# Kernel tuning notes

Measured on AMD Instinct MI355X. Metric: run time of the kernel, lower is better.

Reference implementation:

```python
import jax, jax.numpy as jnp
import numpy as np

N = 100000   # nodes
E = 3200000  # edges
CIN = 6
H = 256
G = 16       # graphs in batch
EPS = 1e-5


def setup_inputs() -> dict:
    key = jax.random.key(0)
    ks = jax.random.split(key, 16)
    inp = {
        'pos': jax.random.normal(ks[0], (N, 3), dtype=jnp.float32),
        'norm': jax.random.normal(ks[1], (N, 3), dtype=jnp.float32),
        'edge_index': jax.random.randint(ks[2], (2, E), 0, N, dtype=jnp.int64),
        'batch': jnp.sort(jax.random.randint(ks[3], (N,), 0, G, dtype=jnp.int64)),
        'bn0_g': jnp.ones((CIN,), jnp.float32), 'bn0_b': jnp.zeros((CIN,), jnp.float32),
    }
    dims = [(CIN, H), (H, H), (H, H), (H, H)]
    for i, (ci, co) in enumerate(dims, start=1):
        inp[f'W{i}'] = jax.random.normal(ks[3 + i], (ci, co), jnp.float32) * 0.05
        inp[f'b{i}'] = jnp.zeros((co,), jnp.float32)
        inp[f'bn{i}_g'] = jnp.ones((co,), jnp.float32)
        inp[f'bn{i}_b'] = jnp.zeros((co,), jnp.float32)
    return inp


def _bn(x, g, b):
    # BatchNorm1d, training mode: biased batch stats over node dim
    m = jnp.mean(x, axis=0)
    v = jnp.var(x, axis=0)
    return (x - m) * jax.lax.rsqrt(v + EPS) * g + b


def _gcn(x, W, bias, row, col, en, sl):
    # GCNConv: linear -> symmetric-normalized aggregation (with self loops) -> +bias
    xw = x @ W                                             # [N, C_out]
    agg = jax.ops.segment_sum(en[:, None] * xw[row], col, num_segments=N)
    return agg + sl[:, None] * xw + bias


def reference(pos, norm, edge_index, batch,
              bn0_g, bn0_b,
              W1, b1, bn1_g, bn1_b,
              W2, b2, bn2_g, bn2_b,
              W3, b3, bn3_g, bn3_b,
              W4, b4, bn4_g, bn4_b):
    row, col = edge_index[0], edge_index[1]
    # gcn_norm with self loops: deg includes +1 self loop weight
    deg = jax.ops.segment_sum(jnp.ones((E,), jnp.float32), col, num_segments=N) + 1.0
    dinv = jax.lax.rsqrt(deg)
    en = dinv[row] * dinv[col]   # edge norm
    sl = dinv * dinv             # self-loop norm

    x = jnp.concatenate([pos, norm], axis=1)   # [N, 6]
    x = _bn(x, bn0_g, bn0_b)
    for (W, b, g, be) in [(W1, b1, bn1_g, bn1_b), (W2, b2, bn2_g, bn2_b),
                          (W3, b3, bn3_g, bn3_b), (W4, b4, bn4_g, bn4_b)]:
        x = _bn(jax.nn.relu(_gcn(x, W, b, row, col, en, sl)), g, be)

    # global mean pool over graph ids
    sums = jax.ops.segment_sum(x, batch, num_segments=G)
    cnt = jax.ops.segment_sum(jnp.ones((N,), jnp.float32), batch, num_segments=G)
    return sums / jnp.maximum(cnt, 1.0)[:, None]
```

## Files before the change

### kernel.cpp

```cpp
#include <hip/hip_runtime.h>
#include <hip/hip_bf16.h>
#include <cstdint>

#define N_NODES 100000
#define NPAD    100032
#define N_EDGES 3200000
#define HID 256
#define NG 16
#define BN_EPS 1e-5f
#define B0 120
#define PB 1024
#define SROWS ((N_NODES + PB - 1) / PB)
#define PBR 128
#define RPR (PB / PBR)
#define FPART 25000

typedef unsigned short u16;
using bf16x8 = __attribute__((ext_vector_type(8))) short;
using f32x4  = __attribute__((ext_vector_type(4))) float;

__device__ __forceinline__ float bf2f(u16 b) {
    return __uint_as_float(((unsigned)b) << 16);
}
__device__ __forceinline__ u16 f2bf(float f) {
    unsigned u = __float_as_uint(f);
    unsigned r = (u + 0x7FFFu + ((u >> 16) & 1u)) >> 16;
    return (u16)r;
}
__device__ __forceinline__ float4 ld_bf16x4(const u16* p) {
    ushort4 u = *reinterpret_cast<const ushort4*>(p);
    float4 f;
    f.x = bf2f(u.x); f.y = bf2f(u.y); f.z = bf2f(u.z); f.w = bf2f(u.w);
    return f;
}

__global__ void k_count(const int* __restrict__ coli, int* __restrict__ cnt) {
    int i = blockIdx.x * blockDim.x + threadIdx.x;
    int st = gridDim.x * blockDim.x;
    for (; i < N_EDGES; i += st) atomicAdd(&cnt[coli[i]], 1);
}

__global__ void k_scan(const int* __restrict__ cnt, int* __restrict__ ptr,
                       int* __restrict__ ptr2, float* __restrict__ dinv) {
    __shared__ int wsum[16];
    const int t = threadIdx.x;
    const int wv = t >> 6;
    const int ln = t & 63;
    int carry = 0;
    for (int base = 0; base < N_NODES; base += 4096) {
        int idx = base + t * 4;
        int v0 = 0, v1 = 0, v2 = 0, v3 = 0;
        if (idx + 3 < N_NODES) {
            int4 q = *reinterpret_cast<const int4*>(&cnt[idx]);
            v0 = q.x; v1 = q.y; v2 = q.z; v3 = q.w;
        } else {
            if (idx + 0 < N_NODES) v0 = cnt[idx + 0];
            if (idx + 1 < N_NODES) v1 = cnt[idx + 1];
            if (idx + 2 < N_NODES) v2 = cnt[idx + 2];
        }
        if (idx + 0 < N_NODES) dinv[idx + 0] = rsqrtf((float)v0 + 1.0f);
        if (idx + 1 < N_NODES) dinv[idx + 1] = rsqrtf((float)v1 + 1.0f);
        if (idx + 2 < N_NODES) dinv[idx + 2] = rsqrtf((float)v2 + 1.0f);
        if (idx + 3 < N_NODES) dinv[idx + 3] = rsqrtf((float)v3 + 1.0f);
        int s = v0 + v1 + v2 + v3;
        int sc = s;
        for (int off = 1; off < 64; off <<= 1) {
            int u = __shfl_up(sc, off);
            if (ln >= off) sc += u;
        }
        if (ln == 63) wsum[wv] = sc;
        __syncthreads();
        if (wv == 0 && ln < 16) {
            int a = wsum[ln];
            for (int off = 1; off < 16; off <<= 1) {
                int u = __shfl_up(a, off, 16);
                if (ln >= off) a += u;
            }
            wsum[ln] = a;
        }
        __syncthreads();
        int total = wsum[15];
        int excl = carry + (wv ? wsum[wv - 1] : 0) + sc - s;
        if (idx + 0 < N_NODES) { ptr[idx + 0] = excl; ptr2[idx + 0] = excl; } excl += v0;
        if (idx + 1 < N_NODES) { ptr[idx + 1] = excl; ptr2[idx + 1] = excl; } excl += v1;
        if (idx + 2 < N_NODES) { ptr[idx + 2] = excl; ptr2[idx + 2] = excl; } excl += v2;
        if (idx + 3 < N_NODES) { ptr[idx + 3] = excl; ptr2[idx + 3] = excl; }
        __syncthreads();
        carry += total;
    }
    if (t == 0) ptr[N_NODES] = carry;
}

__global__ void k_fillp(const int* __restrict__ rowi, const int* __restrict__ coli,
                        int* __restrict__ ptr2, int* __restrict__ esrc, int lo) {
    int i = blockIdx.x * blockDim.x + threadIdx.x;
    int st = gridDim.x * blockDim.x;
    const int hi = lo + FPART;
    for (; i < N_EDGES; i += st) {
        int c = coli[i];
        if (c >= lo && c < hi) {
            int p = atomicAdd(&ptr2[c], 1);
            esrc[p] = rowi[i];
        }
    }
}

__global__ __launch_bounds__(256) void k_batchcnt(const int* __restrict__ batch,
                                                  int* __restrict__ cg) {
    __shared__ int h[NG];
    if (threadIdx.x < NG) h[threadIdx.x] = 0;
    __syncthreads();
    int i = blockIdx.x * blockDim.x + threadIdx.x;
    if (i < N_NODES) atomicAdd(&h[batch[i]], 1);
    __syncthreads();
    if (threadIdx.x < NG) {
        int v = h[threadIdx.x];
        if (v) atomicAdd(&cg[threadIdx.x], v);
    }
}

__global__ __launch_bounds__(256) void k_bn0stats(const float* __restrict__ pos,
                                                  const float* __restrict__ nrm,
                                                  float* __restrict__ part ) {
    float s[6] = {0, 0, 0, 0, 0, 0}, q[6] = {0, 0, 0, 0, 0, 0};
    int i = blockIdx.x * blockDim.x + threadIdx.x;
    int stp = gridDim.x * blockDim.x;
    for (; i < N_NODES; i += stp) {
        float v;
        v = pos[i * 3 + 0]; s[0] += v; q[0] += v * v;
        v = pos[i * 3 + 1]; s[1] += v; q[1] += v * v;
        v = pos[i * 3 + 2]; s[2] += v; q[2] += v * v;
        v = nrm[i * 3 + 0]; s[3] += v; q[3] += v * v;
        v = nrm[i * 3 + 1]; s[4] += v; q[4] += v * v;
        v = nrm[i * 3 + 2]; s[5] += v; q[5] += v * v;
    }
#pragma unroll
    for (int k = 0; k < 6; ++k) {
        for (int o = 32; o > 0; o >>= 1) { s[k] += __shfl_down(s[k], o); q[k] += __shfl_down(q[k], o); }
    }
    __shared__ float ls[4][12];
    const int wv = threadIdx.x >> 6;
    const int ln = threadIdx.x & 63;
    if (ln == 0) {
#pragma unroll
        for (int k = 0; k < 6; ++k) { ls[wv][k] = s[k]; ls[wv][6 + k] = q[k]; }
    }
    __syncthreads();
    if (threadIdx.x < 12)
        part[blockIdx.x * 12 + threadIdx.x] =
            ls[0][threadIdx.x] + ls[1][threadIdx.x] + ls[2][threadIdx.x] + ls[3][threadIdx.x];
}

__global__ void k_fold6(const float* __restrict__ W,
                        const float* __restrict__ part, float invcnt,
                        const float* __restrict__ gamma, const float* __restrict__ beta,
                        float* __restrict__ Wf, float* __restrict__ rvB) {
    __shared__ float st[12];
    int c = threadIdx.x;
    if (c < 12) {
        float a = 0.f;
        for (int b = 0; b < B0; ++b) a += part[b * 12 + c];
        st[c] = a;
    }
    __syncthreads();
    float acc = 0.f;
    for (int k = 0; k < 6; ++k) {
        float m = st[k] * invcnt;
        float var = st[6 + k] * invcnt - m * m;
        float A = gamma[k] * rsqrtf(var + BN_EPS);
        float B = beta[k] - m * A;
        float w = W[k * HID + c];
        Wf[k * HID + c] = A * w;
        acc = fmaf(B, w, acc);
    }
    rvB[c] = acc;
}

__global__ __launch_bounds__(256) void k_reduce(const float* __restrict__ part,
                                                float* __restrict__ red) {
    const int b = blockIdx.x;
    const int t = threadIdx.x;
    float a0 = 0.f, a1 = 0.f;
#pragma unroll
    for (int r = 0; r < RPR; ++r) {
        const float* p = &part[(size_t)(b * RPR + r) * 512];
        a0 += p[t];
        a1 += p[t + 256];
    }
    red[(size_t)b * 512 + t] = a0;
    red[(size_t)b * 512 + 256 + t] = a1;
}

__global__ void k_fold256(const float* __restrict__ W,
                          const float* __restrict__ red , float invcnt,
                          const float* __restrict__ gamma, const float* __restrict__ beta,
                          u16* __restrict__ WhiT, u16* __restrict__ WloT,
                          float* __restrict__ rv) {
    __shared__ float ss[HID], sq[HID];
    int c = threadIdx.x;
    {
        float a = 0.f, b = 0.f;
#pragma unroll 4
        for (int bb = 0; bb < PBR; ++bb) {
            a += red[bb * 512 + c];
            b += red[bb * 512 + HID + c];
        }
        ss[c] = a; sq[c] = b;
    }
    __syncthreads();
    float acc = 0.f;
    for (int k = 0; k < HID; ++k) {
        float m = ss[k] * invcnt;
        float var = sq[k] * invcnt - m * m;
        float A = gamma[k] * rsqrtf(var + BN_EPS);
        float B = beta[k] - m * A;
        float w = W[k * HID + c];
        float wf = A * w;
        u16 hi = f2bf(wf);
        WhiT[c * HID + k] = hi;
        WloT[c * HID + k] = f2bf(wf - bf2f(hi));
        acc = fmaf(B, w, acc);
    }
    rv[c] = acc;
}

__global__ __launch_bounds__(256) void k_agg6(
    const float* __restrict__ pos, const float* __restrict__ nrm,
    const int* __restrict__ ptr, const int* __restrict__ esrc,
    const float* __restrict__ dinv, float* __restrict__ z) {
    const int wv = threadIdx.x >> 6;
    const int ln = threadIdx.x & 63;
    const int n = blockIdx.x * 4 + wv;
    const float dn = dinv[n];
    float z0 = 0, z1 = 0, z2 = 0, z3 = 0, z4 = 0, z5 = 0, t = 0;
    const int s_ = ptr[n], e_ = ptr[n + 1];
    for (int e = s_ + ln; e < e_; e += 64) {
        int src = esrc[e];
        float w = dn * dinv[src];
        z0 = fmaf(w, pos[src * 3 + 0], z0);
        z1 = fmaf(w, pos[src * 3 + 1], z1);
        z2 = fmaf(w, pos[src * 3 + 2], z2);
        z3 = fmaf(w, nrm[src * 3 + 0], z3);
        z4 = fmaf(w, nrm[src * 3 + 1], z4);
        z5 = fmaf(w, nrm[src * 3 + 2], z5);
        t += w;
    }
    if (ln == 0) {
        float sl = dn * dn;
        z0 = fmaf(sl, pos[n * 3 + 0], z0);
        z1 = fmaf(sl, pos[n * 3 + 1], z1);
        z2 = fmaf(sl, pos[n * 3 + 2], z2);
        z3 = fmaf(sl, nrm[n * 3 + 0], z3);
        z4 = fmaf(sl, nrm[n * 3 + 1], z4);
        z5 = fmaf(sl, nrm[n * 3 + 2], z5);
        t += sl;
    }
#pragma unroll
    for (int o = 1; o < 64; o <<= 1) {
        z0 += __shfl_xor(z0, o); z1 += __shfl_xor(z1, o); z2 += __shfl_xor(z2, o);
        z3 += __shfl_xor(z3, o); z4 += __shfl_xor(z4, o); z5 += __shfl_xor(z5, o);
        t  += __shfl_xor(t, o);
    }
    if (ln == 0) {
        *reinterpret_cast<f32x4*>(&z[n * 8])     = f32x4{z0, z1, z2, z3};
        *reinterpret_cast<f32x4*>(&z[n * 8 + 4]) = f32x4{z4, z5, t, 0.f};
    }
}

__global__ __launch_bounds__(256) void k_gemm1b(
    const float* __restrict__ z, const float* __restrict__ Wf,
    const float* __restrict__ rvB, const float* __restrict__ b1,
    u16* __restrict__ out) {
    const int c = threadIdx.x;
    float w0 = Wf[0 * HID + c], w1 = Wf[1 * HID + c], w2 = Wf[2 * HID + c];
    float w3 = Wf[3 * HID + c], w4 = Wf[4 * HID + c], w5 = Wf[5 * HID + c];
    const float rvc = rvB[c], bc = b1[c];
    for (int n = blockIdx.x; n < N_NODES; n += gridDim.x) {
        float x0 = z[n * 8 + 0], x1 = z[n * 8 + 1], x2 = z[n * 8 + 2];
        float x3 = z[n * 8 + 3], x4 = z[n * 8 + 4], x5 = z[n * 8 + 5];
        float s  = z[n * 8 + 6];
        float acc = fmaf(s, rvc, bc);
        acc = fmaf(x0, w0, acc); acc = fmaf(x1, w1, acc); acc = fmaf(x2, w2, acc);
        acc = fmaf(x3, w3, acc); acc = fmaf(x4, w4, acc); acc = fmaf(x5, w5, acc);
        out[(size_t)n * HID + c] = f2bf(fmaxf(acc, 0.f));
    }
}

__global__ __launch_bounds__(256) void k_gemm_mfma(
    const u16* __restrict__ X, const u16* __restrict__ WhiT,
    const u16* __restrict__ WloT, const float* __restrict__ rv,
    u16* __restrict__ out) {
    const int tid = threadIdx.x;
    const int wv = tid >> 6;
    const int ln = tid & 63;
    const int row0 = blockIdx.x * 64;
    const int lr = ln & 15;
    const int lk = (ln >> 4) * 8;
    const int wcol0 = wv * 64;

    f32x4 acc[4][4] = {};
    for (int kk = 0; kk < HID; kk += 32) {
        bf16x8 a[4], bh[4], bl[4];
#pragma unroll
        for (int i = 0; i < 4; ++i) {
            int r = row0 + i * 16 + lr;
            a[i] = *reinterpret_cast<const bf16x8*>(&X[(size_t)r * HID + kk + lk]);
        }
#pragma unroll
        for (int c = 0; c < 4; ++c) {
            int col = wcol0 + c * 16 + lr;
            bh[c] = *reinterpret_cast<const bf16x8*>(&WhiT[(size_t)col * HID + kk + lk]);
            bl[c] = *reinterpret_cast<const bf16x8*>(&WloT[(size_t)col * HID + kk + lk]);
        }
#pragma unroll
        for (int i = 0; i < 4; ++i)
#pragma unroll
            for (int c = 0; c < 4; ++c) {
                acc[i][c] = __builtin_amdgcn_mfma_f32_16x16x32_bf16(a[i], bh[c], acc[i][c], 0, 0, 0);
                acc[i][c] = __builtin_amdgcn_mfma_f32_16x16x32_bf16(a[i], bl[c], acc[i][c], 0, 0, 0);
            }
    }
    const int crow = (ln >> 4) * 4;
#pragma unroll
    for (int c = 0; c < 4; ++c) {
        int col = wcol0 + c * 16 + lr;
        float rvc = rv[col];
#pragma unroll
        for (int i = 0; i < 4; ++i) {
#pragma unroll
            for (int rg = 0; rg < 4; ++rg) {
                int r = row0 + i * 16 + crow + rg;
                out[(size_t)r * HID + col] = f2bf(acc[i][c][rg] + rvc);
            }
        }
    }
}

__global__ __launch_bounds__(256) void k_agg(
    const u16* __restrict__ xw, const int* __restrict__ ptr,
    const int* __restrict__ esrc, const float* __restrict__ dinv,
    const float* __restrict__ bias, u16* __restrict__ y) {
    const int wv = threadIdx.x >> 6;
    const int ln = threadIdx.x & 63;
    const int n = blockIdx.x * 4 + wv;
    const float dn = dinv[n];
    const size_t base = (size_t)n * HID + ln * 4;
    float4 v = ld_bf16x4(&xw[base]);
    const float sl = dn * dn;
    float a0 = v.x * sl, a1 = v.y * sl, a2 = v.z * sl, a3 = v.w * sl;
    const int s = ptr[n], e = ptr[n + 1];
    for (int bs = s; bs < e; bs += 64) {
        const int cnt = (e - bs < 64) ? e - bs : 64;
        int myidx = 0;
        float myw = 0.f;
        if (ln < cnt) {
            myidx = esrc[bs + ln];
            myw = dinv[myidx] * dn;
        }
        int j = 0;
        for (; j + 3 < cnt; j += 4) {
            int   s0 = __shfl(myidx, j),     s1 = __shfl(myidx, j + 1);
            int   s2 = __shfl(myidx, j + 2), s3 = __shfl(myidx, j + 3);
            float w0 = __shfl(myw, j),       w1 = __shfl(myw, j + 1);
            float w2 = __shfl(myw, j + 2),   w3 = __shfl(myw, j + 3);
            float4 u0 = ld_bf16x4(&xw[(size_t)s0 * HID + ln * 4]);
            float4 u1 = ld_bf16x4(&xw[(size_t)s1 * HID + ln * 4]);
            float4 u2 = ld_bf16x4(&xw[(size_t)s2 * HID + ln * 4]);
            float4 u3 = ld_bf16x4(&xw[(size_t)s3 * HID + ln * 4]);
            a0 = fmaf(w0, u0.x, a0); a1 = fmaf(w0, u0.y, a1);
            a2 = fmaf(w0, u0.z, a2); a3 = fmaf(w0, u0.w, a3);
            a0 = fmaf(w1, u1.x, a0); a1 = fmaf(w1, u1.y, a1);
            a2 = fmaf(w1, u1.z, a2); a3 = fmaf(w1, u1.w, a3);
            a0 = fmaf(w2, u2.x, a0); a1 = fmaf(w2, u2.y, a1);
            a2 = fmaf(w2, u2.z, a2); a3 = fmaf(w2, u2.w, a3);
            a0 = fmaf(w3, u3.x, a0); a1 = fmaf(w3, u3.y, a1);
            a2 = fmaf(w3, u3.z, a2); a3 = fmaf(w3, u3.w, a3);
        }
        for (; j < cnt; ++j) {
            int   s0 = __shfl(myidx, j);
            float w0 = __shfl(myw, j);
            float4 u0 = ld_bf16x4(&xw[(size_t)s0 * HID + ln * 4]);
            a0 = fmaf(w0, u0.x, a0); a1 = fmaf(w0, u0.y, a1);
            a2 = fmaf(w0, u0.z, a2); a3 = fmaf(w0, u0.w, a3);
        }
    }
    float4 b = *reinterpret_cast<const float4*>(&bias[ln * 4]);
    a0 = fmaxf(a0 + b.x, 0.f);
    a1 = fmaxf(a1 + b.y, 0.f);
    a2 = fmaxf(a2 + b.z, 0.f);
    a3 = fmaxf(a3 + b.w, 0.f);
    ushort4 o;
    o.x = f2bf(a0); o.y = f2bf(a1); o.z = f2bf(a2); o.w = f2bf(a3);
    *reinterpret_cast<ushort4*>(&y[base]) = o;
}

__global__ __launch_bounds__(256) void k_stats(const u16* __restrict__ y,
                                               float* __restrict__ part ) {
    const int t = threadIdx.x;
    const int cl = t & 63;
    const int rp = t >> 6;
    const int n0 = blockIdx.x * SROWS;
    const int n1 = (n0 + SROWS < N_NODES) ? n0 + SROWS : N_NODES;
    float s0 = 0, s1 = 0, s2 = 0, s3 = 0, q0 = 0, q1 = 0, q2 = 0, q3 = 0;
    for (int n = n0 + rp; n < n1; n += 4) {
        float4 v = ld_bf16x4(&y[(size_t)n * HID + cl * 4]);
        s0 += v.x; q0 = fmaf(v.x, v.x, q0);
        s1 += v.y; q1 = fmaf(v.y, v.y, q1);
        s2 += v.z; q2 = fmaf(v.z, v.z, q2);
        s3 += v.w; q3 = fmaf(v.w, v.w, q3);
    }
    __shared__ float sh[4 * 512];
    float* shr = &sh[rp * 512];
    shr[cl * 4 + 0] = s0; shr[cl * 4 + 1] = s1;
    shr[cl * 4 + 2] = s2; shr[cl * 4 + 3] = s3;
    shr[256 + cl * 4 + 0] = q0; shr[256 + cl * 4 + 1] = q1;
    shr[256 + cl * 4 + 2] = q2; shr[256 + cl * 4 + 3] = q3;
    __syncthreads();
    float a = sh[t] + sh[512 + t] + sh[1024 + t] + sh[1536 + t];
    float b = sh[256 + t] + sh[768 + t] + sh[1280 + t] + sh[1792 + t];
    part[blockIdx.x * 512 + t] = a;
    part[blockIdx.x * 512 + 256 + t] = b;
}

__global__ __launch_bounds__(256) void k_statspool(const u16* __restrict__ y,
                                                   const int* __restrict__ batch,
                                                   float* __restrict__ part,
                                                   float* __restrict__ ps) {
    const int c = threadIdx.x;
    const int n0 = blockIdx.x * SROWS;
    const int n1 = (n0 + SROWS < N_NODES) ? n0 + SROWS : N_NODES;
    float s = 0.f, q = 0.f;
    if (n0 < N_NODES) {
        int cur = batch[n0];
        float acc = 0.f;
        for (int n = n0; n < n1; ++n) {
            float v = bf2f(y[(size_t)n * HID + c]);
            int g = batch[n];
            if (g != cur) {
                atomicAdd(&ps[cur * HID + c], acc);
                acc = 0.f;
                cur = g;
            }
            s += v;
            q = fmaf(v, v, q);
            acc += v;
        }
        atomicAdd(&ps[cur * HID + c], acc);
    }
    part[blockIdx.x * 512 + c] = s;
    part[blockIdx.x * 512 + HID + c] = q;
}

__global__ void k_final(const float* __restrict__ ps, const int* __restrict__ cg,
                        const float* __restrict__ red, const float* __restrict__ gamma,
                        const float* __restrict__ beta, float* __restrict__ out) {
    __shared__ float ss[HID], sq[HID];
    const int c = threadIdx.x;
    {
        float a = 0.f, b = 0.f;
#pragma unroll 4
        for (int bb = 0; bb < PBR; ++bb) {
            a += red[bb * 512 + c];
            b += red[bb * 512 + HID + c];
        }
        ss[c] = a; sq[c] = b;
    }
    __syncthreads();
    const float invn = 1.0f / (float)N_NODES;
    float m = ss[c] * invn;
    float var = sq[c] * invn - m * m;
    float A = gamma[c] * rsqrtf(var + BN_EPS);
    float B = beta[c] - m * A;
    for (int g = 0; g < NG; ++g) {
        float cn = (float)cg[g];
        float val = (A * ps[g * HID + c] + cn * B) / fmaxf(cn, 1.0f);
        out[g * HID + c] = val;
    }
}

extern "C" void kernel_launch(void* const* d_in, const int* in_sizes, int n_in,
                              void* d_out, int out_size, void* d_ws, size_t ws_size,
                              hipStream_t stream) {
    const float* pos   = (const float*)d_in[0];
    const float* nrm   = (const float*)d_in[1];
    const int*   ei    = (const int*)d_in[2];
    const int*   batch = (const int*)d_in[3];
    const float* bn0g  = (const float*)d_in[4];
    const float* bn0b  = (const float*)d_in[5];
    const float* W[4]   = {(const float*)d_in[6],  (const float*)d_in[10], (const float*)d_in[14], (const float*)d_in[18]};
    const float* bb[4]  = {(const float*)d_in[7],  (const float*)d_in[11], (const float*)d_in[15], (const float*)d_in[19]};
    const float* bg[4]  = {(const float*)d_in[8],  (const float*)d_in[12], (const float*)d_in[16], (const float*)d_in[20]};
    const float* bbt[4] = {(const float*)d_in[9],  (const float*)d_in[13], (const float*)d_in[17], (const float*)d_in[21]};

    char* wp = (char*)d_ws;
    auto alloc = [&](size_t bytes) {
        char* p = wp;
        wp += (bytes + 255) & ~(size_t)255;
        return p;
    };
    float* dinv  = (float*)alloc((size_t)N_NODES * 4);
    int*   cnt   = (int*)  alloc((size_t)N_NODES * 4);
    int*   ptr   = (int*)  alloc((size_t)(N_NODES + 1) * 4);
    int*   ptr2  = (int*)  alloc((size_t)N_NODES * 4);
    int*   esrc  = (int*)  alloc((size_t)N_EDGES * 4);
    u16*   bufA  = (u16*)  alloc((size_t)NPAD * HID * 2);
    u16*   bufB  = (u16*)  alloc((size_t)NPAD * HID * 2);
    float* zbuf  = (float*)alloc((size_t)N_NODES * 8 * 4);
    float* part0 = (float*)alloc((size_t)B0 * 12 * 4);
    float* partL = (float*)alloc((size_t)PB * 512 * 4);
    float* red   = (float*)alloc((size_t)PBR * 512 * 4);
    float* Wf1   = (float*)alloc((size_t)6 * HID * 4);
    u16*   WhiT  = (u16*)  alloc((size_t)HID * HID * 2);
    u16*   WloT  = (u16*)  alloc((size_t)HID * HID * 2);
    float* rv    = (float*)alloc(HID * 4);
    float* ps    = (float*)alloc(NG * HID * 4);
    int*   cg    = (int*)  alloc(NG * 4);
    (void)ws_size; (void)in_sizes; (void)n_in; (void)out_size;

    const int* rowi = ei;
    const int* coli = ei + N_EDGES;

    hipMemsetAsync(cnt, 0, (size_t)N_NODES * 4, stream);
    hipMemsetAsync(ps, 0, NG * HID * 4, stream);
    hipMemsetAsync(cg, 0, NG * 4, stream);

    k_count<<<2048, 256, 0, stream>>>(coli, cnt);
    k_scan<<<1, 1024, 0, stream>>>(cnt, ptr, ptr2, dinv);
    for (int p = 0; p < 4; ++p)
        k_fillp<<<1024, 256, 0, stream>>>(rowi, coli, ptr2, esrc, p * FPART);
    k_batchcnt<<<(N_NODES + 255) / 256, 256, 0, stream>>>(batch, cg);

    k_bn0stats<<<B0, 256, 0, stream>>>(pos, nrm, part0);
    k_fold6<<<1, 256, 0, stream>>>(W[0], part0, 1.0f / (float)N_NODES, bn0g, bn0b, Wf1, rv);
    k_agg6<<<N_NODES / 4, 256, 0, stream>>>(pos, nrm, ptr, esrc, dinv, zbuf);
    k_gemm1b<<<2048, 256, 0, stream>>>(zbuf, Wf1, rv, bb[0], bufA);

    for (int l = 0; l < 3; ++l) {
        k_stats<<<PB, 256, 0, stream>>>(bufA, partL);
        k_reduce<<<PBR, 256, 0, stream>>>(partL, red);
        k_fold256<<<1, 256, 0, stream>>>(W[l + 1], red, 1.0f / (float)N_NODES,
                                         bg[l], bbt[l], WhiT, WloT, rv);
        k_gemm_mfma<<<NPAD / 64, 256, 0, stream>>>(bufA, WhiT, WloT, rv, bufB);
        k_agg<<<N_NODES / 4, 256, 0, stream>>>(bufB, ptr, esrc, dinv, bb[l + 1], bufA);
    }

    k_statspool<<<PB, 256, 0, stream>>>(bufA, batch, partL, ps);
    k_reduce<<<PBR, 256, 0, stream>>>(partL, red);
    k_final<<<1, 256, 0, stream>>>(ps, cg, red, bg[3], bbt[3], (float*)d_out);
}
```

Baseline: 1.692 ms.

## Fuse layer-1 aggregation with GEMM, stage GEMM A-tile in LDS, unroll aggregation

Fuses the 6-channel aggregation and the first linear layer into one kernel, so the intermediate z buffer is never written and read back. Folds the batch counting into the BN0 stats kernel and merges two memsets into one. Stages the 64-row A tile in LDS with padded rows before the MFMA loop, and unrolls the neighbor gather in k_agg from 4 to 8 to get more loads in flight. The costs are extra LDS use per block, more registers in the aggregation kernel, and LDS atomics added to the stats kernel.

```diff
diff --git a/kernel.cpp b/kernel.cpp
--- a/kernel.cpp
+++ b/kernel.cpp
@@ -14,6 +14,7 @@
 #define PBR 128
 #define RPR (PB / PBR)
 #define FPART 25000
+#define LDSROW 264
 
 typedef unsigned short u16;
 using bf16x8 = __attribute__((ext_vector_type(8))) short;
@@ -99,29 +100,21 @@
     for (; i < N_EDGES; i += st) {
         int c = coli[i];
         if (c >= lo && c < hi) {
+            int r = rowi[i];
             int p = atomicAdd(&ptr2[c], 1);
-            esrc[p] = rowi[i];
-        }
-    }
-}
-
-__global__ __launch_bounds__(256) void k_batchcnt(const int* __restrict__ batch,
+            esrc[p] = r;
+        }
+    }
+}
+
+__global__ __launch_bounds__(256) void k_bn0stats(const float* __restrict__ pos,
+                                                  const float* __restrict__ nrm,
+                                                  const int* __restrict__ batch,
+                                                  float* __restrict__ part ,
                                                   int* __restrict__ cg) {
     __shared__ int h[NG];
     if (threadIdx.x < NG) h[threadIdx.x] = 0;
     __syncthreads();
-    int i = blockIdx.x * blockDim.x + threadIdx.x;
-    if (i < N_NODES) atomicAdd(&h[batch[i]], 1);
-    __syncthreads();
-    if (threadIdx.x < NG) {
-        int v = h[threadIdx.x];
-        if (v) atomicAdd(&cg[threadIdx.x], v);
-    }
-}
-
-__global__ __launch_bounds__(256) void k_bn0stats(const float* __restrict__ pos,
-                                                  const float* __restrict__ nrm,
-                                                  float* __restrict__ part ) {
     float s[6] = {0, 0, 0, 0, 0, 0}, q[6] = {0, 0, 0, 0, 0, 0};
     int i = blockIdx.x * blockDim.x + threadIdx.x;
     int stp = gridDim.x * blockDim.x;
@@ -133,6 +126,7 @@
         v = nrm[i * 3 + 0]; s[3] += v; q[3] += v * v;
         v = nrm[i * 3 + 1]; s[4] += v; q[4] += v * v;
         v = nrm[i * 3 + 2]; s[5] += v; q[5] += v * v;
+        atomicAdd(&h[batch[i]], 1);
     }
 #pragma unroll
     for (int k = 0; k < 6; ++k) {
@@ -149,6 +143,10 @@
     if (threadIdx.x < 12)
         part[blockIdx.x * 12 + threadIdx.x] =
             ls[0][threadIdx.x] + ls[1][threadIdx.x] + ls[2][threadIdx.x] + ls[3][threadIdx.x];
+    if (threadIdx.x < NG) {
+        int v = h[threadIdx.x];
+        if (v) atomicAdd(&cg[threadIdx.x], v);
+    }
 }
 
 __global__ void k_fold6(const float* __restrict__ W,
@@ -224,72 +222,84 @@
     rv[c] = acc;
 }
 
-__global__ __launch_bounds__(256) void k_agg6(
+__global__ __launch_bounds__(256) void k_l1fused(
     const float* __restrict__ pos, const float* __restrict__ nrm,
     const int* __restrict__ ptr, const int* __restrict__ esrc,
-    const float* __restrict__ dinv, float* __restrict__ z) {
+    const float* __restrict__ dinv, const float* __restrict__ Wf,
+    const float* __restrict__ rvB, const float* __restrict__ b1,
+    u16* __restrict__ out) {
     const int wv = threadIdx.x >> 6;
     const int ln = threadIdx.x & 63;
-    const int n = blockIdx.x * 4 + wv;
-    const float dn = dinv[n];
-    float z0 = 0, z1 = 0, z2 = 0, z3 = 0, z4 = 0, z5 = 0, t = 0;
-    const int s_ = ptr[n], e_ = ptr[n + 1];
-    for (int e = s_ + ln; e < e_; e += 64) {
-        int src = esrc[e];
-        float w = dn * dinv[src];
-        z0 = fmaf(w, pos[src * 3 + 0], z0);
-        z1 = fmaf(w, pos[src * 3 + 1], z1);
-        z2 = fmaf(w, pos[src * 3 + 2], z2);
-        z3 = fmaf(w, nrm[src * 3 + 0], z3);
-        z4 = fmaf(w, nrm[src * 3 + 1], z4);
-        z5 = fmaf(w, nrm[src * 3 + 2], z5);
-        t += w;
-    }
-    if (ln == 0) {
-        float sl = dn * dn;
-        z0 = fmaf(sl, pos[n * 3 + 0], z0);
-        z1 = fmaf(sl, pos[n * 3 + 1], z1);
-        z2 = fmaf(sl, pos[n * 3 + 2], z2);
-        z3 = fmaf(sl, nrm[n * 3 + 0], z3);
-        z4 = fmaf(sl, nrm[n * 3 + 1], z4);
-        z5 = fmaf(sl, nrm[n * 3 + 2], z5);
-        t += sl;
-    }
-#pragma unroll
-    for (int o = 1; o < 64; o <<= 1) {
-        z0 += __shfl_xor(z0, o); z1 += __shfl_xor(z1, o); z2 += __shfl_xor(z2, o);
-        z3 += __shfl_xor(z3, o); z4 += __shfl_xor(z4, o); z5 += __shfl_xor(z5, o);
-        t  += __shfl_xor(t, o);
-    }
-    if (ln == 0) {
-        *reinterpret_cast<f32x4*>(&z[n * 8])     = f32x4{z0, z1, z2, z3};
-        *reinterpret_cast<f32x4*>(&z[n * 8 + 4]) = f32x4{z4, z5, t, 0.f};
-    }
-}
-
-__global__ __launch_bounds__(256) void k_gemm1b(
-    const float* __restrict__ z, const float* __restrict__ Wf,
-    const float* __restrict__ rvB, const float* __restrict__ b1,
-    u16* __restrict__ out) {
-    const int c = threadIdx.x;
-    float w0 = Wf[0 * HID + c], w1 = Wf[1 * HID + c], w2 = Wf[2 * HID + c];
-    float w3 = Wf[3 * HID + c], w4 = Wf[4 * HID + c], w5 = Wf[5 * HID + c];
-    const float rvc = rvB[c], bc = b1[c];
-    for (int n = blockIdx.x; n < N_NODES; n += gridDim.x) {
-        float x0 = z[n * 8 + 0], x1 = z[n * 8 + 1], x2 = z[n * 8 + 2];
-        float x3 = z[n * 8 + 3], x4 = z[n * 8 + 4], x5 = z[n * 8 + 5];
-        float s  = z[n * 8 + 6];
-        float acc = fmaf(s, rvc, bc);
-        acc = fmaf(x0, w0, acc); acc = fmaf(x1, w1, acc); acc = fmaf(x2, w2, acc);
-        acc = fmaf(x3, w3, acc); acc = fmaf(x4, w4, acc); acc = fmaf(x5, w5, acc);
-        out[(size_t)n * HID + c] = f2bf(fmaxf(acc, 0.f));
-    }
-}
-
-__global__ __launch_bounds__(256) void k_gemm_mfma(
+    float w[6][4], rv4[4], bb4[4];
+#pragma unroll
+    for (int k = 0; k < 6; ++k) {
+        float4 t = *reinterpret_cast<const float4*>(&Wf[k * HID + ln * 4]);
+        w[k][0] = t.x; w[k][1] = t.y; w[k][2] = t.z; w[k][3] = t.w;
+    }
+    {
+        float4 t = *reinterpret_cast<const float4*>(&rvB[ln * 4]);
+        rv4[0] = t.x; rv4[1] = t.y; rv4[2] = t.z; rv4[3] = t.w;
+        float4 u = *reinterpret_cast<const float4*>(&b1[ln * 4]);
+        bb4[0] = u.x; bb4[1] = u.y; bb4[2] = u.z; bb4[3] = u.w;
+    }
+    for (int n = blockIdx.x * 4 + wv; n < N_NODES; n += gridDim.x * 4) {
+        const float dn = dinv[n];
+        float z0 = 0, z1 = 0, z2 = 0, z3 = 0, z4 = 0, z5 = 0, t = 0;
+        const int s_ = ptr[n], e_ = ptr[n + 1];
+        for (int e = s_ + ln; e < e_; e += 64) {
+            int src = esrc[e];
+            float we = dn * dinv[src];
+            z0 = fmaf(we, pos[src * 3 + 0], z0);
+            z1 = fmaf(we, pos[src * 3 + 1], z1);
+            z2 = fmaf(we, pos[src * 3 + 2], z2);
+            z3 = fmaf(we, nrm[src * 3 + 0], z3);
+            z4 = fmaf(we, nrm[src * 3 + 1], z4);
+            z5 = fmaf(we, nrm[src * 3 + 2], z5);
+            t += we;
+        }
+        if (ln == 0) {
+            float sl = dn * dn;
+            z0 = fmaf(sl, pos[n * 3 + 0], z0);
+            z1 = fmaf(sl, pos[n * 3 + 1], z1);
+            z2 = fmaf(sl, pos[n * 3 + 2], z2);
+            z3 = fmaf(sl, nrm[n * 3 + 0], z3);
+            z4 = fmaf(sl, nrm[n * 3 + 1], z4);
+            z5 = fmaf(sl, nrm[n * 3 + 2], z5);
+            t += sl;
+        }
+#pragma unroll
+        for (int o = 1; o < 64; o <<= 1) {
+            z0 += __shfl_xor(z0, o); z1 += __shfl_xor(z1, o); z2 += __shfl_xor(z2, o);
+            z3 += __shfl_xor(z3, o); z4 += __shfl_xor(z4, o); z5 += __shfl_xor(z5, o);
+            t  += __shfl_xor(t, o);
+        }
+        ushort4 o4;
+        float oj;
+        oj = fmaf(t, rv4[0], bb4[0]);
+        oj = fmaf(z0, w[0][0], oj); oj = fmaf(z1, w[1][0], oj); oj = fmaf(z2, w[2][0], oj);
+        oj = fmaf(z3, w[3][0], oj); oj = fmaf(z4, w[4][0], oj); oj = fmaf(z5, w[5][0], oj);
+        o4.x = f2bf(fmaxf(oj, 0.f));
+        oj = fmaf(t, rv4[1], bb4[1]);
+        oj = fmaf(z0, w[0][1], oj); oj = fmaf(z1, w[1][1], oj); oj = fmaf(z2, w[2][1], oj);
+        oj = fmaf(z3, w[3][1], oj); oj = fmaf(z4, w[4][1], oj); oj = fmaf(z5, w[5][1], oj);
+        o4.y = f2bf(fmaxf(oj, 0.f));
+        oj = fmaf(t, rv4[2], bb4[2]);
+        oj = fmaf(z0, w[0][2], oj); oj = fmaf(z1, w[1][2], oj); oj = fmaf(z2, w[2][2], oj);
+        oj = fmaf(z3, w[3][2], oj); oj = fmaf(z4, w[4][2], oj); oj = fmaf(z5, w[5][2], oj);
+        o4.z = f2bf(fmaxf(oj, 0.f));
+        oj = fmaf(t, rv4[3], bb4[3]);
+        oj = fmaf(z0, w[0][3], oj); oj = fmaf(z1, w[1][3], oj); oj = fmaf(z2, w[2][3], oj);
+        oj = fmaf(z3, w[3][3], oj); oj = fmaf(z4, w[4][3], oj); oj = fmaf(z5, w[5][3], oj);
+        o4.w = f2bf(fmaxf(oj, 0.f));
+        *reinterpret_cast<ushort4*>(&out[(size_t)n * HID + ln * 4]) = o4;
+    }
+}
+
+__global__ __launch_bounds__(256) void k_gemm_lds(
     const u16* __restrict__ X, const u16* __restrict__ WhiT,
     const u16* __restrict__ WloT, const float* __restrict__ rv,
     u16* __restrict__ out) {
+    __shared__ u16 As[64 * LDSROW];
     const int tid = threadIdx.x;
     const int wv = tid >> 6;
     const int ln = tid & 63;
@@ -298,14 +308,22 @@
     const int lk = (ln >> 4) * 8;
     const int wcol0 = wv * 64;
 
+#pragma unroll
+    for (int i = 0; i < 8; ++i) {
+        int chunk = i * 256 + tid;
+        int r = chunk >> 5;
+        int kc = chunk & 31;
+        bf16x8 v = *reinterpret_cast<const bf16x8*>(&X[(size_t)(row0 + r) * HID + kc * 8]);
+        *reinterpret_cast<bf16x8*>(&As[r * LDSROW + kc * 8]) = v;
+    }
+    __syncthreads();
+
     f32x4 acc[4][4] = {};
     for (int kk = 0; kk < HID; kk += 32) {
         bf16x8 a[4], bh[4], bl[4];
 #pragma unroll
-        for (int i = 0; i < 4; ++i) {
-            int r = row0 + i * 16 + lr;
-            a[i] = *reinterpret_cast<const bf16x8*>(&X[(size_t)r * HID + kk + lk]);
-        }
+        for (int i = 0; i < 4; ++i)
+            a[i] = *reinterpret_cast<const bf16x8*>(&As[(i * 16 + lr) * LDSROW + kk + lk]);
 #pragma unroll
         for (int c = 0; c < 4; ++c) {
             int col = wcol0 + c * 16 + lr;
@@ -358,15 +376,23 @@
             myw = dinv[myidx] * dn;
         }
         int j = 0;
-        for (; j + 3 < cnt; j += 4) {
+        for (; j + 7 < cnt; j += 8) {
             int   s0 = __shfl(myidx, j),     s1 = __shfl(myidx, j + 1);
             int   s2 = __shfl(myidx, j + 2), s3 = __shfl(myidx, j + 3);
+            int   s4 = __shfl(myidx, j + 4), s5 = __shfl(myidx, j + 5);
+            int   s6 = __shfl(myidx, j + 6), s7 = __shfl(myidx, j + 7);
             float w0 = __shfl(myw, j),       w1 = __shfl(myw, j + 1);
             float w2 = __shfl(myw, j + 2),   w3 = __shfl(myw, j + 3);
+            float w4 = __shfl(myw, j + 4),   w5 = __shfl(myw, j + 5);
+            float w6 = __shfl(myw, j + 6),   w7 = __shfl(myw, j + 7);
             float4 u0 = ld_bf16x4(&xw[(size_t)s0 * HID + ln * 4]);
             float4 u1 = ld_bf16x4(&xw[(size_t)s1 * HID + ln * 4]);
             float4 u2 = ld_bf16x4(&xw[(size_t)s2 * HID + ln * 4]);
             float4 u3 = ld_bf16x4(&xw[(size_t)s3 * HID + ln * 4]);
+            float4 u4 = ld_bf16x4(&xw[(size_t)s4 * HID + ln * 4]);
+            float4 u5 = ld_bf16x4(&xw[(size_t)s5 * HID + ln * 4]);
+            float4 u6 = ld_bf16x4(&xw[(size_t)s6 * HID + ln * 4]);
+            float4 u7 = ld_bf16x4(&xw[(size_t)s7 * HID + ln * 4]);
             a0 = fmaf(w0, u0.x, a0); a1 = fmaf(w0, u0.y, a1);
             a2 = fmaf(w0, u0.z, a2); a3 = fmaf(w0, u0.w, a3);
             a0 = fmaf(w1, u1.x, a0); a1 = fmaf(w1, u1.y, a1);
@@ -375,6 +401,14 @@
             a2 = fmaf(w2, u2.z, a2); a3 = fmaf(w2, u2.w, a3);
             a0 = fmaf(w3, u3.x, a0); a1 = fmaf(w3, u3.y, a1);
             a2 = fmaf(w3, u3.z, a2); a3 = fmaf(w3, u3.w, a3);
+            a0 = fmaf(w4, u4.x, a0); a1 = fmaf(w4, u4.y, a1);
+            a2 = fmaf(w4, u4.z, a2); a3 = fmaf(w4, u4.w, a3);
+            a0 = fmaf(w5, u5.x, a0); a1 = fmaf(w5, u5.y, a1);
+            a2 = fmaf(w5, u5.z, a2); a3 = fmaf(w5, u5.w, a3);
+            a0 = fmaf(w6, u6.x, a0); a1 = fmaf(w6, u6.y, a1);
+            a2 = fmaf(w6, u6.z, a2); a3 = fmaf(w6, u6.w, a3);
+            a0 = fmaf(w7, u7.x, a0); a1 = fmaf(w7, u7.y, a1);
+            a2 = fmaf(w7, u7.z, a2); a3 = fmaf(w7, u7.w, a3);
         }
         for (; j < cnt; ++j) {
             int   s0 = __shfl(myidx, j);
@@ -505,7 +539,6 @@
     int*   esrc  = (int*)  alloc((size_t)N_EDGES * 4);
     u16*   bufA  = (u16*)  alloc((size_t)NPAD * HID * 2);
     u16*   bufB  = (u16*)  alloc((size_t)NPAD * HID * 2);
-    float* zbuf  = (float*)alloc((size_t)N_NODES * 8 * 4);
     float* part0 = (float*)alloc((size_t)B0 * 12 * 4);
     float* partL = (float*)alloc((size_t)PB * 512 * 4);
     float* red   = (float*)alloc((size_t)PBR * 512 * 4);
@@ -513,34 +546,32 @@
     u16*   WhiT  = (u16*)  alloc((size_t)HID * HID * 2);
     u16*   WloT  = (u16*)  alloc((size_t)HID * HID * 2);
     float* rv    = (float*)alloc(HID * 4);
-    float* ps    = (float*)alloc(NG * HID * 4);
-    int*   cg    = (int*)  alloc(NG * 4);
+    float* psz   = (float*)alloc((size_t)(NG * HID + NG) * 4);
+    float* ps    = psz;
+    int*   cg    = (int*)(psz + NG * HID);
     (void)ws_size; (void)in_sizes; (void)n_in; (void)out_size;
 
     const int* rowi = ei;
     const int* coli = ei + N_EDGES;
 
     hipMemsetAsync(cnt, 0, (size_t)N_NODES * 4, stream);
-    hipMemsetAsync(ps, 0, NG * HID * 4, stream);
-    hipMemsetAsync(cg, 0, NG * 4, stream);
+    hipMemsetAsync(psz, 0, (size_t)(NG * HID + NG) * 4, stream);
 
     k_count<<<2048, 256, 0, stream>>>(coli, cnt);
     k_scan<<<1, 1024, 0, stream>>>(cnt, ptr, ptr2, dinv);
     for (int p = 0; p < 4; ++p)
         k_fillp<<<1024, 256, 0, stream>>>(rowi, coli, ptr2, esrc, p * FPART);
-    k_batchcnt<<<(N_NODES + 255) / 256, 256, 0, stream>>>(batch, cg);
-
-    k_bn0stats<<<B0, 256, 0, stream>>>(pos, nrm, part0);
+
+    k_bn0stats<<<B0, 256, 0, stream>>>(pos, nrm, batch, part0, cg);
     k_fold6<<<1, 256, 0, stream>>>(W[0], part0, 1.0f / (float)N_NODES, bn0g, bn0b, Wf1, rv);
-    k_agg6<<<N_NODES / 4, 256, 0, stream>>>(pos, nrm, ptr, esrc, dinv, zbuf);
-    k_gemm1b<<<2048, 256, 0, stream>>>(zbuf, Wf1, rv, bb[0], bufA);
+    k_l1fused<<<2048, 256, 0, stream>>>(pos, nrm, ptr, esrc, dinv, Wf1, rv, bb[0], bufA);
 
     for (int l = 0; l < 3; ++l) {
         k_stats<<<PB, 256, 0, stream>>>(bufA, partL);
         k_reduce<<<PBR, 256, 0, stream>>>(partL, red);
         k_fold256<<<1, 256, 0, stream>>>(W[l + 1], red, 1.0f / (float)N_NODES,
                                          bg[l], bbt[l], WhiT, WloT, rv);
-        k_gemm_mfma<<<NPAD / 64, 256, 0, stream>>>(bufA, WhiT, WloT, rv, bufB);
+        k_gemm_lds<<<NPAD / 64, 256, 0, stream>>>(bufA, WhiT, WloT, rv, bufB);
         k_agg<<<N_NODES / 4, 256, 0, stream>>>(bufB, ptr, esrc, dinv, bb[l + 1], bufA);
     }
 
```

After: 1.615 ms. 1.05x faster.
